# Kernel tuning notes

Hardware: AMD Instinct MI355X
Metric: run time of the kernel (lower is better)

The kernel has to match this reference:

```python
import jax, jax.numpy as jnp
import numpy as np
from functools import partial

D_MODEL, D_STATE, D_CONV, EXPAND = 1024, 16, 4, 2
D_INNER = D_MODEL * EXPAND
B_SZ, L = 4, 2048


def setup_inputs() -> dict:
    key = jax.random.key(0)
    ks = jax.random.split(key, 8)
    s = 0.02
    A_init = jnp.log(jnp.arange(1, D_STATE + 1, dtype=jnp.float32))
    return {
        "x": jax.random.normal(ks[0], (B_SZ, L, D_MODEL), jnp.float32),
        "norm_w": jnp.ones((D_MODEL,), jnp.float32),
        "norm_b": jnp.zeros((D_MODEL,), jnp.float32),
        "W_in": jax.random.normal(ks[1], (D_MODEL, 2 * D_INNER), jnp.float32) * s,
        "conv_w": jax.random.normal(ks[2], (D_INNER, 1, D_CONV), jnp.float32) * 0.3,
        "conv_b": jnp.zeros((D_INNER,), jnp.float32),
        "A_log": jnp.broadcast_to(A_init, (D_INNER, D_STATE)).copy(),
        "W_b": jax.random.normal(ks[3], (D_INNER, D_STATE), jnp.float32) * s,
        "W_c": jax.random.normal(ks[4], (D_INNER, D_STATE), jnp.float32) * s,
        "W_delta": jax.random.normal(ks[5], (D_INNER, D_INNER), jnp.float32) * s,
        "b_delta": jnp.zeros((D_INNER,), jnp.float32),
        "D_param": jnp.ones((D_INNER,), jnp.float32),
        "W_out": jax.random.normal(ks[6], (D_INNER, D_MODEL), jnp.float32) * s,
    }


def _layernorm(x, w, b, eps=1e-5):
    mu = jnp.mean(x, axis=-1, keepdims=True)
    var = jnp.mean(jnp.square(x - mu), axis=-1, keepdims=True)
    return (x - mu) * jax.lax.rsqrt(var + eps) * w + b


def reference(x, norm_w, norm_b, W_in, conv_w, conv_b, A_log, W_b, W_c,
              W_delta, b_delta, D_param, W_out):
    residual = x
    xn = _layernorm(x, norm_w, norm_b)
    xz = jnp.einsum('bld,de->ble', xn, W_in)  # [B, L, 2*D_inner]
    x_path, z = jnp.split(xz, 2, axis=-1)

    # depthwise causal conv1d (torch pads both sides K-1 then slices [:L] == left-pad K-1)
    xc = jnp.moveaxis(x_path, 1, 2)  # [B, D_inner, L]
    xc = jax.lax.conv_general_dilated(
        xc, conv_w, window_strides=(1,), padding=[(D_CONV - 1, 0)],
        dimension_numbers=('NCH', 'OIH', 'NCH'), feature_group_count=D_INNER)
    xc = xc + conv_b[None, :, None]
    x_path = jax.nn.silu(jnp.moveaxis(xc, 2, 1))  # [B, L, D_inner]

    Bm = jnp.einsum('bld,dn->bln', x_path, W_b)   # [B, L, N]
    Cm = jnp.einsum('bld,dn->bln', x_path, W_c)   # [B, L, N]
    delta = jax.nn.softplus(jnp.einsum('bld,de->ble', x_path, W_delta) + b_delta)
    A = -jnp.exp(A_log)  # [D_inner, N]

    def step(h, inp):
        xt, dt, Bt, Ct = inp  # xt,dt: [B,D]; Bt,Ct: [B,N]
        A_bar = jnp.exp(dt[..., None] * A)              # [B, D, N]
        h = A_bar * h + (dt * xt)[..., None] * Bt[:, None, :]
        y = jnp.einsum('bdn,bn->bd', h, Ct) + D_param * xt
        return h, y

    h0 = jnp.zeros((x.shape[0], D_INNER, D_STATE), x_path.dtype)
    xs = (jnp.moveaxis(x_path, 1, 0), jnp.moveaxis(delta, 1, 0),
          jnp.moveaxis(Bm, 1, 0), jnp.moveaxis(Cm, 1, 0))
    _, ys = jax.lax.scan(step, h0, xs)           # ys: [L, B, D_inner]
    y = jnp.moveaxis(ys, 0, 1)                   # [B, L, D_inner]

    return jnp.einsum('bld,de->ble', y * jax.nn.silu(z), W_out) + residual
```

## Files before the change

kernel.cpp:

```cpp
#include <hip/hip_runtime.h>
#include <hip/hip_bf16.h>

#define D_MODEL 1024
#define D_STATE 16
#define D_INNER 2048
#define BSZ     4
#define SEQ     2048
#define NTOK    (BSZ*SEQ)
#define NBIG    2176
#define NCH     16
#define TC      128

typedef __attribute__((ext_vector_type(8))) short short8;
typedef __attribute__((ext_vector_type(4))) float floatx4;

__device__ __forceinline__ ushort bf2us(float f)
{
    union { __hip_bfloat16 h; ushort u; } c;
    c.h = __float2bfloat16(f);
    return c.u;
}
__device__ __forceinline__ float us2f(ushort u)
{
    union { uint u; float f; } c;
    c.u = ((uint)u) << 16;
    return c.f;
}
__device__ __forceinline__ uint pk2(float a, float b)
{
    return (uint)bf2us(a) | ((uint)bf2us(b) << 16);
}
__device__ __forceinline__ float blo(uint u) { return __uint_as_float(u << 16); }
__device__ __forceinline__ float bhi(uint u) { return __uint_as_float(u & 0xffff0000u); }
__device__ __forceinline__ float softplus_f(float v)
{
    return (v > 20.f) ? v : __logf(1.f + __expf(v));
}

__device__ __forceinline__ void load_lds16(const __hip_bfloat16* g, __hip_bfloat16* l)
{
    __builtin_amdgcn_global_load_lds(
        (const __attribute__((address_space(1))) char*)g,
        (__attribute__((address_space(3))) char*)l, 16, 0, 0);
}

__global__ __launch_bounds__(256) void ln_kernel(
    const float* __restrict__ x, const float* __restrict__ w,
    const float* __restrict__ bvec, __hip_bfloat16* __restrict__ out)
{
    int token = blockIdx.x;
    int tid = threadIdx.x;
    const float4 v = ((const float4*)(x + (size_t)token * D_MODEL))[tid];
    float s  = v.x + v.y + v.z + v.w;
    float sq = v.x*v.x + v.y*v.y + v.z*v.z + v.w*v.w;
#pragma unroll
    for (int o = 32; o; o >>= 1) { s += __shfl_down(s, o, 64); sq += __shfl_down(sq, o, 64); }
    __shared__ float red[8];
    int wid = tid >> 6;
    if ((tid & 63) == 0) { red[wid] = s; red[wid + 4] = sq; }
    __syncthreads();
    s  = red[0] + red[1] + red[2] + red[3];
    sq = red[4] + red[5] + red[6] + red[7];
    float mu  = s * (1.f / D_MODEL);
    float var = sq * (1.f / D_MODEL) - mu * mu;
    float rs  = rsqrtf(var + 1e-5f);
    float4 wv = ((const float4*)w)[tid];
    float4 bv = ((const float4*)bvec)[tid];
    union { ushort4 u; __hip_bfloat16 h[4]; } p;
    p.h[0] = __float2bfloat16((v.x - mu) * rs * wv.x + bv.x);
    p.h[1] = __float2bfloat16((v.y - mu) * rs * wv.y + bv.y);
    p.h[2] = __float2bfloat16((v.z - mu) * rs * wv.z + bv.z);
    p.h[3] = __float2bfloat16((v.w - mu) * rs * wv.w + bv.w);
    ((ushort4*)(out + (size_t)token * D_MODEL))[tid] = p.u;
}

__global__ __launch_bounds__(256) void transpose_cast(
    const float* __restrict__ src, __hip_bfloat16* __restrict__ dst,
    int R, int C, int dstStride, int dstRowOff)
{
    __shared__ float tile[32][33];
    int tx = threadIdx.x, ty = threadIdx.y;
    int bx = blockIdx.x, by = blockIdx.y;
#pragma unroll
    for (int i = 0; i < 4; ++i) {
        int r = by * 32 + ty + i * 8;
        int c = bx * 32 + tx;
        if (r < R && c < C) tile[ty + i * 8][tx] = src[(size_t)r * C + c];
    }
    __syncthreads();
#pragma unroll
    for (int i = 0; i < 4; ++i) {
        int c = bx * 32 + ty + i * 8;
        int r = by * 32 + tx;
        if (c < C && r < R)
            dst[(size_t)(dstRowOff + c) * dstStride + r] = __float2bfloat16(tile[tx][ty + i * 8]);
    }
}

__global__ __launch_bounds__(256) void zero_fill(uint4* __restrict__ p, int n)
{
    int i = blockIdx.x * 256 + threadIdx.x;
    if (i < n) { uint4 z = {0, 0, 0, 0}; p[i] = z; }
}

template <int MODE>
__global__ __launch_bounds__(256) void gemm_bt(
    const __hip_bfloat16* __restrict__ A, const __hip_bfloat16* __restrict__ BT,
    int M, int N, int K,
    float* __restrict__ outF,
    __hip_bfloat16* __restrict__ outB1, __hip_bfloat16* __restrict__ outB2,
    const float* __restrict__ extra)
{
    __shared__ __align__(16) __hip_bfloat16 As[128 * 64];
    __shared__ __align__(16) __hip_bfloat16 Bs[128 * 64];
    int tid = threadIdx.x;
    int m0 = blockIdx.x * 128;
    int n0 = blockIdx.y * 128;
    int wv = tid >> 6, lane = tid & 63;
    int wm = (wv >> 1) * 64, wn = (wv & 1) * 64;
    int lr = lane & 15, lq = lane >> 4;

    int srow = wv * 8 + (lane >> 3);
    int scg  = (lane & 7) ^ (lane >> 3);
    const __hip_bfloat16* Ag = A  + (size_t)(m0 + srow) * K + scg * 8;
    const __hip_bfloat16* Bg = BT + (size_t)(n0 + srow) * K + scg * 8;
    __hip_bfloat16* AsW = As + (wv * 8) * 64;
    __hip_bfloat16* BsW = Bs + (wv * 8) * 64;

    int swz = lq ^ (lr & 7);

    floatx4 acc[4][4] = {};

    for (int k0 = 0; k0 < K; k0 += 64) {
        __syncthreads();
#pragma unroll
        for (int i = 0; i < 4; ++i) {
            load_lds16(Ag + (size_t)(i * 32) * K + k0, AsW + i * 32 * 64);
            load_lds16(Bg + (size_t)(i * 32) * K + k0, BsW + i * 32 * 64);
        }
        __syncthreads();
#pragma unroll
        for (int kk = 0; kk < 2; ++kk) {
            int cofs = (swz ^ (kk << 2)) * 8;
            short8 af[4], bf[4];
#pragma unroll
            for (int mi = 0; mi < 4; ++mi)
                af[mi] = *(const short8*)(As + (wm + mi * 16 + lr) * 64 + cofs);
#pragma unroll
            for (int ni = 0; ni < 4; ++ni)
                bf[ni] = *(const short8*)(Bs + (wn + ni * 16 + lr) * 64 + cofs);
#pragma unroll
            for (int mi = 0; mi < 4; ++mi)
#pragma unroll
                for (int ni = 0; ni < 4; ++ni)
                    acc[mi][ni] = __builtin_amdgcn_mfma_f32_16x16x32_bf16(af[mi], bf[ni], acc[mi][ni], 0, 0, 0);
        }
    }

#pragma unroll
    for (int mi = 0; mi < 4; ++mi)
#pragma unroll
        for (int ni = 0; ni < 4; ++ni)
#pragma unroll
            for (int r = 0; r < 4; ++r) {
                int rg = m0 + wm + mi * 16 + lq * 4 + r;
                int cg = n0 + wn + ni * 16 + lr;
                float v = acc[mi][ni][r];
                if (MODE == 1) {
                    if (cg < D_INNER) {
                        outB1[(size_t)rg * D_INNER + cg] = __float2bfloat16(v);
                    } else {
                        float sv = v / (1.f + __expf(-v));
                        outB2[(size_t)rg * D_INNER + (cg - D_INNER)] = __float2bfloat16(sv);
                    }
                } else if (MODE == 2) {
                    if (cg < D_INNER) {
                        outB1[(size_t)rg * D_INNER + cg] = __float2bfloat16(softplus_f(v + extra[cg]));
                    } else if (cg < D_INNER + 32) {
                        outB2[(size_t)rg * 32 + (cg - D_INNER)] = __float2bfloat16(v);
                    }
                } else {
                    outF[(size_t)rg * D_MODEL + cg] = v + extra[(size_t)rg * D_MODEL + cg];
                }
            }
}

__global__ __launch_bounds__(256) void conv_silu(
    const __hip_bfloat16* __restrict__ xin, const float* __restrict__ cw,
    const float* __restrict__ cb, __hip_bfloat16* __restrict__ xp)
{
    int gid = blockIdx.x * 256 + threadIdx.x;
    int d = gid & (D_INNER - 1);
    int rest = gid >> 11;
    int b = rest & 3;
    int ch = rest >> 2;
    int t0 = ch * 64;
    float w0 = cw[d * 4 + 0], w1 = cw[d * 4 + 1], w2 = cw[d * 4 + 2], w3 = cw[d * 4 + 3];
    float bias = cb[d];
    const __hip_bfloat16* base = xin + (size_t)b * SEQ * D_INNER + d;
    __hip_bfloat16* ob = xp + (size_t)b * SEQ * D_INNER + d;
    float xm3 = (t0 >= 3) ? __bfloat162float(base[(size_t)(t0 - 3) * D_INNER]) : 0.f;
    float xm2 = (t0 >= 2) ? __bfloat162float(base[(size_t)(t0 - 2) * D_INNER]) : 0.f;
    float xm1 = (t0 >= 1) ? __bfloat162float(base[(size_t)(t0 - 1) * D_INNER]) : 0.f;
#pragma unroll 4
    for (int t = t0; t < t0 + 64; ++t) {
        float xcur = __bfloat162float(base[(size_t)t * D_INNER]);
        float v = bias + w0 * xm3 + w1 * xm2 + w2 * xm1 + w3 * xcur;
        float sv = v / (1.f + __expf(-v));
        ob[(size_t)t * D_INNER] = __float2bfloat16(sv);
        xm3 = xm2; xm2 = xm1; xm1 = xcur;
    }
}


#define LOAD_A16() \
    const float4* Ar = (const float4*)(A_log + (size_t)d * D_STATE); \
    float4 aA = Ar[0], aB = Ar[1], aC = Ar[2], aD = Ar[3]; \
    float A0 = -__expf(aA.x), A1 = -__expf(aA.y), A2 = -__expf(aA.z), A3 = -__expf(aA.w); \
    float A4 = -__expf(aB.x), A5 = -__expf(aB.y), A6 = -__expf(aB.z), A7 = -__expf(aB.w); \
    float A8 = -__expf(aC.x), A9 = -__expf(aC.y), A10 = -__expf(aC.z), A11 = -__expf(aC.w); \
    float A12 = -__expf(aD.x), A13 = -__expf(aD.y), A14 = -__expf(aD.z), A15 = -__expf(aD.w)

#define UNPACK16(P, r0, r1) \
    float P##0 = blo(r0.x), P##1 = bhi(r0.x), P##2 = blo(r0.y), P##3 = bhi(r0.y); \
    float P##4 = blo(r0.z), P##5 = bhi(r0.z), P##6 = blo(r0.w), P##7 = bhi(r0.w); \
    float P##8 = blo(r1.x), P##9 = bhi(r1.x), P##10 = blo(r1.y), P##11 = bhi(r1.y); \
    float P##12 = blo(r1.z), P##13 = bhi(r1.z), P##14 = blo(r1.w), P##15 = bhi(r1.w)

__global__ __launch_bounds__(256) void scan_p1(
    const ushort* __restrict__ dtb, const ushort* __restrict__ xpb,
    const ushort* __restrict__ BC, const float* __restrict__ A_log,
    ushort* __restrict__ hloc, ushort* __restrict__ prod)
{
    int gid = blockIdx.x * 256 + threadIdx.x;
    int d  = gid & (D_INNER - 1);
    int ch = (gid >> 11) & (NCH - 1);
    int b  = gid >> 15;
    LOAD_A16();
    float h0 = 0.f, h1 = 0.f, h2 = 0.f, h3 = 0.f, h4 = 0.f, h5 = 0.f, h6 = 0.f, h7 = 0.f;
    float h8 = 0.f, h9 = 0.f, h10 = 0.f, h11 = 0.f, h12 = 0.f, h13 = 0.f, h14 = 0.f, h15 = 0.f;
    float dtsum = 0.f;
    size_t mBase = (size_t)b * SEQ + (size_t)ch * TC;
    const ushort* dtp = dtb + mBase * D_INNER + d;
    const ushort* xpp = xpb + mBase * D_INNER + d;
    const uint4*  bcp = (const uint4*)(BC + mBase * 32);
    for (int t = 0; t < TC; ++t) {
        float dt = us2f(dtp[(size_t)t * D_INNER]);
        float xt = us2f(xpp[(size_t)t * D_INNER]);
        uint4 r0 = bcp[t * 4 + 0];
        uint4 r1 = bcp[t * 4 + 1];
        float dtx = dt * xt;
        dtsum += dt;
        UNPACK16(B, r0, r1);
        h0  = __expf(dt * A0)  * h0  + dtx * B0;
        h1  = __expf(dt * A1)  * h1  + dtx * B1;
        h2  = __expf(dt * A2)  * h2  + dtx * B2;
        h3  = __expf(dt * A3)  * h3  + dtx * B3;
        h4  = __expf(dt * A4)  * h4  + dtx * B4;
        h5  = __expf(dt * A5)  * h5  + dtx * B5;
        h6  = __expf(dt * A6)  * h6  + dtx * B6;
        h7  = __expf(dt * A7)  * h7  + dtx * B7;
        h8  = __expf(dt * A8)  * h8  + dtx * B8;
        h9  = __expf(dt * A9)  * h9  + dtx * B9;
        h10 = __expf(dt * A10) * h10 + dtx * B10;
        h11 = __expf(dt * A11) * h11 + dtx * B11;
        h12 = __expf(dt * A12) * h12 + dtx * B12;
        h13 = __expf(dt * A13) * h13 + dtx * B13;
        h14 = __expf(dt * A14) * h14 + dtx * B14;
        h15 = __expf(dt * A15) * h15 + dtx * B15;
    }
    size_t idx = ((size_t)(b * NCH + ch) * D_INNER + d) * D_STATE;
    uint4 ho, h2v, po, p2v;
    ho.x  = pk2(h0, h1);   ho.y  = pk2(h2, h3);
    ho.z  = pk2(h4, h5);   ho.w  = pk2(h6, h7);
    h2v.x = pk2(h8, h9);   h2v.y = pk2(h10, h11);
    h2v.z = pk2(h12, h13); h2v.w = pk2(h14, h15);
    po.x  = pk2(__expf(dtsum * A0),  __expf(dtsum * A1));
    po.y  = pk2(__expf(dtsum * A2),  __expf(dtsum * A3));
    po.z  = pk2(__expf(dtsum * A4),  __expf(dtsum * A5));
    po.w  = pk2(__expf(dtsum * A6),  __expf(dtsum * A7));
    p2v.x = pk2(__expf(dtsum * A8),  __expf(dtsum * A9));
    p2v.y = pk2(__expf(dtsum * A10), __expf(dtsum * A11));
    p2v.z = pk2(__expf(dtsum * A12), __expf(dtsum * A13));
    p2v.w = pk2(__expf(dtsum * A14), __expf(dtsum * A15));
    ((uint4*)(hloc + idx))[0] = ho; ((uint4*)(hloc + idx))[1] = h2v;
    ((uint4*)(prod + idx))[0] = po; ((uint4*)(prod + idx))[1] = p2v;
}

__global__ __launch_bounds__(256) void scan_mid(
    ushort* __restrict__ hloc, const ushort* __restrict__ prod)
{
    int gid = blockIdx.x * 256 + threadIdx.x;
    int n = gid & 15, d = (gid >> 4) & (D_INNER - 1), b = gid >> 15;
    float h = 0.f;
#pragma unroll
    for (int ch = 0; ch < NCH; ++ch) {
        size_t idx = ((size_t)(b * NCH + ch) * D_INNER + d) * D_STATE + n;
        float old = us2f(hloc[idx]);
        float p   = us2f(prod[idx]);
        hloc[idx] = bf2us(h);
        h = old + p * h;
    }
}

__global__ __launch_bounds__(256) void scan_p2(
    const ushort* __restrict__ dtb, const ushort* __restrict__ xpb,
    const ushort* __restrict__ BC, const float* __restrict__ A_log,
    const float* __restrict__ D_param, const ushort* __restrict__ hin,
    ushort* __restrict__ zio)
{
    int gid = blockIdx.x * 256 + threadIdx.x;
    int d  = gid & (D_INNER - 1);
    int ch = (gid >> 11) & (NCH - 1);
    int b  = gid >> 15;
    LOAD_A16();
    float Dp = D_param[d];
    size_t idx = ((size_t)(b * NCH + ch) * D_INNER + d) * D_STATE;
    uint4 hr0 = ((const uint4*)(hin + idx))[0];
    uint4 hr1 = ((const uint4*)(hin + idx))[1];
    float h0 = blo(hr0.x), h1 = bhi(hr0.x), h2 = blo(hr0.y), h3 = bhi(hr0.y);
    float h4 = blo(hr0.z), h5 = bhi(hr0.z), h6 = blo(hr0.w), h7 = bhi(hr0.w);
    float h8 = blo(hr1.x), h9 = bhi(hr1.x), h10 = blo(hr1.y), h11 = bhi(hr1.y);
    float h12 = blo(hr1.z), h13 = bhi(hr1.z), h14 = blo(hr1.w), h15 = bhi(hr1.w);
    size_t mBase = (size_t)b * SEQ + (size_t)ch * TC;
    const ushort* dtp = dtb + mBase * D_INNER + d;
    const ushort* xpp = xpb + mBase * D_INNER + d;
    const uint4*  bcp = (const uint4*)(BC + mBase * 32);
    ushort* zp = zio + mBase * D_INNER + d;
    for (int t = 0; t < TC; ++t) {
        float dt = us2f(dtp[(size_t)t * D_INNER]);
        float xt = us2f(xpp[(size_t)t * D_INNER]);
        uint4 r0 = bcp[t * 4 + 0];
        uint4 r1 = bcp[t * 4 + 1];
        uint4 r2 = bcp[t * 4 + 2];
        uint4 r3 = bcp[t * 4 + 3];
        UNPACK16(B, r0, r1);
        UNPACK16(C, r2, r3);
        float dtx = dt * xt;
        float y = Dp * xt;
        h0  = __expf(dt * A0)  * h0  + dtx * B0;   y += h0  * C0;
        h1  = __expf(dt * A1)  * h1  + dtx * B1;   y += h1  * C1;
        h2  = __expf(dt * A2)  * h2  + dtx * B2;   y += h2  * C2;
        h3  = __expf(dt * A3)  * h3  + dtx * B3;   y += h3  * C3;
        h4  = __expf(dt * A4)  * h4  + dtx * B4;   y += h4  * C4;
        h5  = __expf(dt * A5)  * h5  + dtx * B5;   y += h5  * C5;
        h6  = __expf(dt * A6)  * h6  + dtx * B6;   y += h6  * C6;
        h7  = __expf(dt * A7)  * h7  + dtx * B7;   y += h7  * C7;
        h8  = __expf(dt * A8)  * h8  + dtx * B8;   y += h8  * C8;
        h9  = __expf(dt * A9)  * h9  + dtx * B9;   y += h9  * C9;
        h10 = __expf(dt * A10) * h10 + dtx * B10;  y += h10 * C10;
        h11 = __expf(dt * A11) * h11 + dtx * B11;  y += h11 * C11;
        h12 = __expf(dt * A12) * h12 + dtx * B12;  y += h12 * C12;
        h13 = __expf(dt * A13) * h13 + dtx * B13;  y += h13 * C13;
        h14 = __expf(dt * A14) * h14 + dtx * B14;  y += h14 * C14;
        h15 = __expf(dt * A15) * h15 + dtx * B15;  y += h15 * C15;
        float z = us2f(zp[(size_t)t * D_INNER]);
        zp[(size_t)t * D_INNER] = bf2us(y * z);
    }
}

extern "C" void kernel_launch(void* const* d_in, const int* in_sizes, int n_in,
                              void* d_out, int out_size, void* d_ws, size_t ws_size,
                              hipStream_t stream)
{
    const float* x       = (const float*)d_in[0];
    const float* norm_w  = (const float*)d_in[1];
    const float* norm_b  = (const float*)d_in[2];
    const float* W_in    = (const float*)d_in[3];
    const float* conv_w  = (const float*)d_in[4];
    const float* conv_b  = (const float*)d_in[5];
    const float* A_log   = (const float*)d_in[6];
    const float* W_b     = (const float*)d_in[7];
    const float* W_c     = (const float*)d_in[8];
    const float* W_delta = (const float*)d_in[9];
    const float* b_delta = (const float*)d_in[10];
    const float* D_param = (const float*)d_in[11];
    const float* W_out   = (const float*)d_in[12];
    float* out = (float*)d_out;

    char* ws = (char*)d_ws;
    char* R1 = ws;
    char* R2 = R1 + (size_t)33554432;
    char* R3 = R2 + (size_t)33554432;
    char* R4 = R3 + (size_t)33554432;
    char* R5 = R4 + (size_t)8912896;

    __hip_bfloat16* xnb  = (__hip_bfloat16*)R1;
    __hip_bfloat16* wT1  = (__hip_bfloat16*)(R1 + 16777216);
    __hip_bfloat16* xp   = (__hip_bfloat16*)R1;
    __hip_bfloat16* xraw = (__hip_bfloat16*)R2;
    __hip_bfloat16* dtb  = (__hip_bfloat16*)R2;
    __hip_bfloat16* wT3  = (__hip_bfloat16*)R2;
    __hip_bfloat16* zio  = (__hip_bfloat16*)R3;
    __hip_bfloat16* wT2  = (__hip_bfloat16*)R4;
    ushort*         hloc = (ushort*)R4;
    ushort*         prodb= (ushort*)(R4 + 4194304);
    __hip_bfloat16* BCb  = (__hip_bfloat16*)R5;

    ln_kernel<<<NTOK, 256, 0, stream>>>(x, norm_w, norm_b, xnb);

    transpose_cast<<<dim3(128, 32), dim3(32, 8), 0, stream>>>(W_in, wT1, 1024, 4096, 1024, 0);

    gemm_bt<1><<<dim3(NTOK / 128, 4096 / 128), 256, 0, stream>>>(
        xnb, wT1, NTOK, 4096, 1024, nullptr, xraw, zio, nullptr);

    transpose_cast<<<dim3(64, 64), dim3(32, 8), 0, stream>>>(W_delta, wT2, 2048, 2048, 2048, 0);
    transpose_cast<<<dim3(1, 64),  dim3(32, 8), 0, stream>>>(W_b,     wT2, 2048, 16,   2048, 2048);
    transpose_cast<<<dim3(1, 64),  dim3(32, 8), 0, stream>>>(W_c,     wT2, 2048, 16,   2048, 2064);
    zero_fill<<<96, 256, 0, stream>>>((uint4*)(wT2 + (size_t)2080 * 2048), 24576);

    conv_silu<<<1024, 256, 0, stream>>>(xraw, conv_w, conv_b, xp);

    gemm_bt<2><<<dim3(NTOK / 128, NBIG / 128), 256, 0, stream>>>(
        xp, wT2, NTOK, NBIG, 2048, nullptr, dtb, BCb, b_delta);

    scan_p1<<<512, 256, 0, stream>>>((const ushort*)dtb, (const ushort*)xp,
                                     (const ushort*)BCb, A_log, hloc, prodb);
    scan_mid<<<512, 256, 0, stream>>>(hloc, prodb);
    scan_p2<<<512, 256, 0, stream>>>((const ushort*)dtb, (const ushort*)xp,
                                     (const ushort*)BCb, A_log, D_param, hloc,
                                     (ushort*)zio);

    transpose_cast<<<dim3(32, 64), dim3(32, 8), 0, stream>>>(W_out, wT3, 2048, 1024, 2048, 0);

    gemm_bt<3><<<dim3(NTOK / 128, D_MODEL / 128), 256, 0, stream>>>(
        zio, wT3, NTOK, D_MODEL, 2048, out, nullptr, nullptr, x);

    (void)in_sizes; (void)n_in; (void)out_size; (void)ws_size;
}
```

Measured before the change: 582.5 us.

## Fuse weight prep kernels, fold chunk-prefix into scan_p2, prefetch scan inputs

```diff
diff --git a/kernel.cpp b/kernel.cpp
--- a/kernel.cpp
+++ b/kernel.cpp
@@ -74,13 +74,11 @@
     ((ushort4*)(out + (size_t)token * D_MODEL))[tid] = p.u;
 }
 
-__global__ __launch_bounds__(256) void transpose_cast(
+__device__ __forceinline__ void tr_body(
     const float* __restrict__ src, __hip_bfloat16* __restrict__ dst,
-    int R, int C, int dstStride, int dstRowOff)
+    int R, int C, int dstStride, int dstRowOff, int bx, int by, int tx, int ty)
 {
     __shared__ float tile[32][33];
-    int tx = threadIdx.x, ty = threadIdx.y;
-    int bx = blockIdx.x, by = blockIdx.y;
 #pragma unroll
     for (int i = 0; i < 4; ++i) {
         int r = by * 32 + ty + i * 8;
@@ -97,14 +95,39 @@
     }
 }
 
-__global__ __launch_bounds__(256) void zero_fill(uint4* __restrict__ p, int n)
-{
-    int i = blockIdx.x * 256 + threadIdx.x;
-    if (i < n) { uint4 z = {0, 0, 0, 0}; p[i] = z; }
+__global__ __launch_bounds__(256) void transpose_cast(
+    const float* __restrict__ src, __hip_bfloat16* __restrict__ dst,
+    int R, int C, int dstStride, int dstRowOff)
+{
+    tr_body(src, dst, R, C, dstStride, dstRowOff,
+            blockIdx.x, blockIdx.y, threadIdx.x, threadIdx.y);
+}
+
+__global__ __launch_bounds__(256) void prep_w(
+    const float* __restrict__ W_in, const float* __restrict__ W_delta,
+    const float* __restrict__ W_b, const float* __restrict__ W_c,
+    __hip_bfloat16* __restrict__ wT1, __hip_bfloat16* __restrict__ wT2)
+{
+    int s = blockIdx.x;
+    int tx = threadIdx.x, ty = threadIdx.y;
+    if (s < 4096) {
+        tr_body(W_in, wT1, 1024, 4096, 1024, 0, s & 127, s >> 7, tx, ty);
+    } else if (s < 8192) {
+        int q = s - 4096;
+        tr_body(W_delta, wT2, 2048, 2048, 2048, 0, q & 63, q >> 6, tx, ty);
+    } else if (s < 8256) {
+        tr_body(W_b, wT2, 2048, 16, 2048, 2048, 0, s - 8192, tx, ty);
+    } else if (s < 8320) {
+        tr_body(W_c, wT2, 2048, 16, 2048, 2064, 0, s - 8256, tx, ty);
+    } else {
+        int i = (s - 8320) * 256 + ty * 32 + tx;
+        uint4 z = {0, 0, 0, 0};
+        ((uint4*)(wT2 + (size_t)2080 * 2048))[i] = z;
+    }
 }
 
 template <int MODE>
-__global__ __launch_bounds__(256) void gemm_bt(
+__device__ __forceinline__ void gemm_body(
     const __hip_bfloat16* __restrict__ A, const __hip_bfloat16* __restrict__ BT,
     int M, int N, int K,
     float* __restrict__ outF,
@@ -185,6 +208,27 @@
             }
 }
 
+__global__ __launch_bounds__(256) void gemm_xz(
+    const __hip_bfloat16* __restrict__ A, const __hip_bfloat16* __restrict__ BT,
+    int M, int N, int K, float* __restrict__ outF,
+    __hip_bfloat16* __restrict__ o1, __hip_bfloat16* __restrict__ o2,
+    const float* __restrict__ extra)
+{ gemm_body<1>(A, BT, M, N, K, outF, o1, o2, extra); }
+
+__global__ __launch_bounds__(256) void gemm_dbc(
+    const __hip_bfloat16* __restrict__ A, const __hip_bfloat16* __restrict__ BT,
+    int M, int N, int K, float* __restrict__ outF,
+    __hip_bfloat16* __restrict__ o1, __hip_bfloat16* __restrict__ o2,
+    const float* __restrict__ extra)
+{ gemm_body<2>(A, BT, M, N, K, outF, o1, o2, extra); }
+
+__global__ __launch_bounds__(256) void gemm_out(
+    const __hip_bfloat16* __restrict__ A, const __hip_bfloat16* __restrict__ BT,
+    int M, int N, int K, float* __restrict__ outF,
+    __hip_bfloat16* __restrict__ o1, __hip_bfloat16* __restrict__ o2,
+    const float* __restrict__ extra)
+{ gemm_body<3>(A, BT, M, N, K, outF, o1, o2, extra); }
+
 __global__ __launch_bounds__(256) void conv_silu(
     const __hip_bfloat16* __restrict__ xin, const float* __restrict__ cw,
     const float* __restrict__ cb, __hip_bfloat16* __restrict__ xp)
@@ -227,6 +271,26 @@
     float P##8 = blo(r1.x), P##9 = bhi(r1.x), P##10 = blo(r1.y), P##11 = bhi(r1.y); \
     float P##12 = blo(r1.z), P##13 = bhi(r1.z), P##14 = blo(r1.w), P##15 = bhi(r1.w)
 
+#define SCAN_STEP_B() do { \
+    float dtx = dt * xt; \
+    h0  = __expf(dt * A0)  * h0  + dtx * B0; \
+    h1  = __expf(dt * A1)  * h1  + dtx * B1; \
+    h2  = __expf(dt * A2)  * h2  + dtx * B2; \
+    h3  = __expf(dt * A3)  * h3  + dtx * B3; \
+    h4  = __expf(dt * A4)  * h4  + dtx * B4; \
+    h5  = __expf(dt * A5)  * h5  + dtx * B5; \
+    h6  = __expf(dt * A6)  * h6  + dtx * B6; \
+    h7  = __expf(dt * A7)  * h7  + dtx * B7; \
+    h8  = __expf(dt * A8)  * h8  + dtx * B8; \
+    h9  = __expf(dt * A9)  * h9  + dtx * B9; \
+    h10 = __expf(dt * A10) * h10 + dtx * B10; \
+    h11 = __expf(dt * A11) * h11 + dtx * B11; \
+    h12 = __expf(dt * A12) * h12 + dtx * B12; \
+    h13 = __expf(dt * A13) * h13 + dtx * B13; \
+    h14 = __expf(dt * A14) * h14 + dtx * B14; \
+    h15 = __expf(dt * A15) * h15 + dtx * B15; \
+} while (0)
+
 __global__ __launch_bounds__(256) void scan_p1(
     const ushort* __restrict__ dtb, const ushort* __restrict__ xpb,
     const ushort* __restrict__ BC, const float* __restrict__ A_log,
@@ -244,30 +308,25 @@
     const ushort* dtp = dtb + mBase * D_INNER + d;
     const ushort* xpp = xpb + mBase * D_INNER + d;
     const uint4*  bcp = (const uint4*)(BC + mBase * 32);
-    for (int t = 0; t < TC; ++t) {
-        float dt = us2f(dtp[(size_t)t * D_INNER]);
-        float xt = us2f(xpp[(size_t)t * D_INNER]);
-        uint4 r0 = bcp[t * 4 + 0];
-        uint4 r1 = bcp[t * 4 + 1];
-        float dtx = dt * xt;
+    float dt = us2f(dtp[0]);
+    float xt = us2f(xpp[0]);
+    uint4 r0 = bcp[0], r1 = bcp[1];
+    for (int t = 0; t < TC - 1; ++t) {
+        float dt_n = us2f(dtp[(size_t)(t + 1) * D_INNER]);
+        float xt_n = us2f(xpp[(size_t)(t + 1) * D_INNER]);
+        uint4 r0_n = bcp[(t + 1) * 4 + 0];
+        uint4 r1_n = bcp[(t + 1) * 4 + 1];
+        {
+            UNPACK16(B, r0, r1);
+            dtsum += dt;
+            SCAN_STEP_B();
+        }
+        dt = dt_n; xt = xt_n; r0 = r0_n; r1 = r1_n;
+    }
+    {
+        UNPACK16(B, r0, r1);
         dtsum += dt;
-        UNPACK16(B, r0, r1);
-        h0  = __expf(dt * A0)  * h0  + dtx * B0;
-        h1  = __expf(dt * A1)  * h1  + dtx * B1;
-        h2  = __expf(dt * A2)  * h2  + dtx * B2;
-        h3  = __expf(dt * A3)  * h3  + dtx * B3;
-        h4  = __expf(dt * A4)  * h4  + dtx * B4;
-        h5  = __expf(dt * A5)  * h5  + dtx * B5;
-        h6  = __expf(dt * A6)  * h6  + dtx * B6;
-        h7  = __expf(dt * A7)  * h7  + dtx * B7;
-        h8  = __expf(dt * A8)  * h8  + dtx * B8;
-        h9  = __expf(dt * A9)  * h9  + dtx * B9;
-        h10 = __expf(dt * A10) * h10 + dtx * B10;
-        h11 = __expf(dt * A11) * h11 + dtx * B11;
-        h12 = __expf(dt * A12) * h12 + dtx * B12;
-        h13 = __expf(dt * A13) * h13 + dtx * B13;
-        h14 = __expf(dt * A14) * h14 + dtx * B14;
-        h15 = __expf(dt * A15) * h15 + dtx * B15;
+        SCAN_STEP_B();
     }
     size_t idx = ((size_t)(b * NCH + ch) * D_INNER + d) * D_STATE;
     uint4 ho, h2v, po, p2v;
@@ -287,27 +346,11 @@
     ((uint4*)(prod + idx))[0] = po; ((uint4*)(prod + idx))[1] = p2v;
 }
 
-__global__ __launch_bounds__(256) void scan_mid(
-    ushort* __restrict__ hloc, const ushort* __restrict__ prod)
-{
-    int gid = blockIdx.x * 256 + threadIdx.x;
-    int n = gid & 15, d = (gid >> 4) & (D_INNER - 1), b = gid >> 15;
-    float h = 0.f;
-#pragma unroll
-    for (int ch = 0; ch < NCH; ++ch) {
-        size_t idx = ((size_t)(b * NCH + ch) * D_INNER + d) * D_STATE + n;
-        float old = us2f(hloc[idx]);
-        float p   = us2f(prod[idx]);
-        hloc[idx] = bf2us(h);
-        h = old + p * h;
-    }
-}
-
 __global__ __launch_bounds__(256) void scan_p2(
     const ushort* __restrict__ dtb, const ushort* __restrict__ xpb,
     const ushort* __restrict__ BC, const float* __restrict__ A_log,
-    const float* __restrict__ D_param, const ushort* __restrict__ hin,
-    ushort* __restrict__ zio)
+    const float* __restrict__ D_param, const ushort* __restrict__ hloc,
+    const ushort* __restrict__ prod, ushort* __restrict__ zio)
 {
     int gid = blockIdx.x * 256 + threadIdx.x;
     int d  = gid & (D_INNER - 1);
@@ -315,47 +358,67 @@
     int b  = gid >> 15;
     LOAD_A16();
     float Dp = D_param[d];
-    size_t idx = ((size_t)(b * NCH + ch) * D_INNER + d) * D_STATE;
-    uint4 hr0 = ((const uint4*)(hin + idx))[0];
-    uint4 hr1 = ((const uint4*)(hin + idx))[1];
-    float h0 = blo(hr0.x), h1 = bhi(hr0.x), h2 = blo(hr0.y), h3 = bhi(hr0.y);
-    float h4 = blo(hr0.z), h5 = bhi(hr0.z), h6 = blo(hr0.w), h7 = bhi(hr0.w);
-    float h8 = blo(hr1.x), h9 = bhi(hr1.x), h10 = blo(hr1.y), h11 = bhi(hr1.y);
-    float h12 = blo(hr1.z), h13 = bhi(hr1.z), h14 = blo(hr1.w), h15 = bhi(hr1.w);
+    float h0 = 0.f, h1 = 0.f, h2 = 0.f, h3 = 0.f, h4 = 0.f, h5 = 0.f, h6 = 0.f, h7 = 0.f;
+    float h8 = 0.f, h9 = 0.f, h10 = 0.f, h11 = 0.f, h12 = 0.f, h13 = 0.f, h14 = 0.f, h15 = 0.f;
+    for (int j = 0; j < ch; ++j) {
+        size_t jdx = ((size_t)(b * NCH + j) * D_INNER + d) * D_STATE;
+        uint4 a0 = ((const uint4*)(hloc + jdx))[0];
+        uint4 a1 = ((const uint4*)(hloc + jdx))[1];
+        uint4 q0 = ((const uint4*)(prod + jdx))[0];
+        uint4 q1 = ((const uint4*)(prod + jdx))[1];
+        h0  = blo(a0.x) + blo(q0.x) * h0;   h1  = bhi(a0.x) + bhi(q0.x) * h1;
+        h2  = blo(a0.y) + blo(q0.y) * h2;   h3  = bhi(a0.y) + bhi(q0.y) * h3;
+        h4  = blo(a0.z) + blo(q0.z) * h4;   h5  = bhi(a0.z) + bhi(q0.z) * h5;
+        h6  = blo(a0.w) + blo(q0.w) * h6;   h7  = bhi(a0.w) + bhi(q0.w) * h7;
+        h8  = blo(a1.x) + blo(q1.x) * h8;   h9  = bhi(a1.x) + bhi(q1.x) * h9;
+        h10 = blo(a1.y) + blo(q1.y) * h10;  h11 = bhi(a1.y) + bhi(q1.y) * h11;
+        h12 = blo(a1.z) + blo(q1.z) * h12;  h13 = bhi(a1.z) + bhi(q1.z) * h13;
+        h14 = blo(a1.w) + blo(q1.w) * h14;  h15 = bhi(a1.w) + bhi(q1.w) * h15;
+    }
     size_t mBase = (size_t)b * SEQ + (size_t)ch * TC;
     const ushort* dtp = dtb + mBase * D_INNER + d;
     const ushort* xpp = xpb + mBase * D_INNER + d;
     const uint4*  bcp = (const uint4*)(BC + mBase * 32);
     ushort* zp = zio + mBase * D_INNER + d;
+    float dt = us2f(dtp[0]);
+    float xt = us2f(xpp[0]);
+    uint4 r0 = bcp[0], r1 = bcp[1], r2 = bcp[2], r3 = bcp[3];
     for (int t = 0; t < TC; ++t) {
-        float dt = us2f(dtp[(size_t)t * D_INNER]);
-        float xt = us2f(xpp[(size_t)t * D_INNER]);
-        uint4 r0 = bcp[t * 4 + 0];
-        uint4 r1 = bcp[t * 4 + 1];
-        uint4 r2 = bcp[t * 4 + 2];
-        uint4 r3 = bcp[t * 4 + 3];
-        UNPACK16(B, r0, r1);
-        UNPACK16(C, r2, r3);
-        float dtx = dt * xt;
-        float y = Dp * xt;
-        h0  = __expf(dt * A0)  * h0  + dtx * B0;   y += h0  * C0;
-        h1  = __expf(dt * A1)  * h1  + dtx * B1;   y += h1  * C1;
-        h2  = __expf(dt * A2)  * h2  + dtx * B2;   y += h2  * C2;
-        h3  = __expf(dt * A3)  * h3  + dtx * B3;   y += h3  * C3;
-        h4  = __expf(dt * A4)  * h4  + dtx * B4;   y += h4  * C4;
-        h5  = __expf(dt * A5)  * h5  + dtx * B5;   y += h5  * C5;
-        h6  = __expf(dt * A6)  * h6  + dtx * B6;   y += h6  * C6;
-        h7  = __expf(dt * A7)  * h7  + dtx * B7;   y += h7  * C7;
-        h8  = __expf(dt * A8)  * h8  + dtx * B8;   y += h8  * C8;
-        h9  = __expf(dt * A9)  * h9  + dtx * B9;   y += h9  * C9;
-        h10 = __expf(dt * A10) * h10 + dtx * B10;  y += h10 * C10;
-        h11 = __expf(dt * A11) * h11 + dtx * B11;  y += h11 * C11;
-        h12 = __expf(dt * A12) * h12 + dtx * B12;  y += h12 * C12;
-        h13 = __expf(dt * A13) * h13 + dtx * B13;  y += h13 * C13;
-        h14 = __expf(dt * A14) * h14 + dtx * B14;  y += h14 * C14;
-        h15 = __expf(dt * A15) * h15 + dtx * B15;  y += h15 * C15;
-        float z = us2f(zp[(size_t)t * D_INNER]);
-        zp[(size_t)t * D_INNER] = bf2us(y * z);
+        float dt_n = 0.f, xt_n = 0.f;
+        uint4 r0_n = {0,0,0,0}, r1_n = {0,0,0,0}, r2_n = {0,0,0,0}, r3_n = {0,0,0,0};
+        if (t < TC - 1) {
+            dt_n = us2f(dtp[(size_t)(t + 1) * D_INNER]);
+            xt_n = us2f(xpp[(size_t)(t + 1) * D_INNER]);
+            r0_n = bcp[(t + 1) * 4 + 0];
+            r1_n = bcp[(t + 1) * 4 + 1];
+            r2_n = bcp[(t + 1) * 4 + 2];
+            r3_n = bcp[(t + 1) * 4 + 3];
+        }
+        {
+            UNPACK16(B, r0, r1);
+            UNPACK16(C, r2, r3);
+            float dtx = dt * xt;
+            float y = Dp * xt;
+            h0  = __expf(dt * A0)  * h0  + dtx * B0;   y += h0  * C0;
+            h1  = __expf(dt * A1)  * h1  + dtx * B1;   y += h1  * C1;
+            h2  = __expf(dt * A2)  * h2  + dtx * B2;   y += h2  * C2;
+            h3  = __expf(dt * A3)  * h3  + dtx * B3;   y += h3  * C3;
+            h4  = __expf(dt * A4)  * h4  + dtx * B4;   y += h4  * C4;
+            h5  = __expf(dt * A5)  * h5  + dtx * B5;   y += h5  * C5;
+            h6  = __expf(dt * A6)  * h6  + dtx * B6;   y += h6  * C6;
+            h7  = __expf(dt * A7)  * h7  + dtx * B7;   y += h7  * C7;
+            h8  = __expf(dt * A8)  * h8  + dtx * B8;   y += h8  * C8;
+            h9  = __expf(dt * A9)  * h9  + dtx * B9;   y += h9  * C9;
+            h10 = __expf(dt * A10) * h10 + dtx * B10;  y += h10 * C10;
+            h11 = __expf(dt * A11) * h11 + dtx * B11;  y += h11 * C11;
+            h12 = __expf(dt * A12) * h12 + dtx * B12;  y += h12 * C12;
+            h13 = __expf(dt * A13) * h13 + dtx * B13;  y += h13 * C13;
+            h14 = __expf(dt * A14) * h14 + dtx * B14;  y += h14 * C14;
+            h15 = __expf(dt * A15) * h15 + dtx * B15;  y += h15 * C15;
+            float z = us2f(zp[(size_t)t * D_INNER]);
+            zp[(size_t)t * D_INNER] = bf2us(y * z);
+        }
+        dt = dt_n; xt = xt_n; r0 = r0_n; r1 = r1_n; r2 = r2_n; r3 = r3_n;
     }
 }
 
@@ -399,31 +462,25 @@
 
     ln_kernel<<<NTOK, 256, 0, stream>>>(x, norm_w, norm_b, xnb);
 
-    transpose_cast<<<dim3(128, 32), dim3(32, 8), 0, stream>>>(W_in, wT1, 1024, 4096, 1024, 0);
-
-    gemm_bt<1><<<dim3(NTOK / 128, 4096 / 128), 256, 0, stream>>>(
+    prep_w<<<8416, dim3(32, 8), 0, stream>>>(W_in, W_delta, W_b, W_c, wT1, wT2);
+
+    gemm_xz<<<dim3(NTOK / 128, 4096 / 128), 256, 0, stream>>>(
         xnb, wT1, NTOK, 4096, 1024, nullptr, xraw, zio, nullptr);
 
-    transpose_cast<<<dim3(64, 64), dim3(32, 8), 0, stream>>>(W_delta, wT2, 2048, 2048, 2048, 0);
-    transpose_cast<<<dim3(1, 64),  dim3(32, 8), 0, stream>>>(W_b,     wT2, 2048, 16,   2048, 2048);
-    transpose_cast<<<dim3(1, 64),  dim3(32, 8), 0, stream>>>(W_c,     wT2, 2048, 16,   2048, 2064);
-    zero_fill<<<96, 256, 0, stream>>>((uint4*)(wT2 + (size_t)2080 * 2048), 24576);
-
     conv_silu<<<1024, 256, 0, stream>>>(xraw, conv_w, conv_b, xp);
 
-    gemm_bt<2><<<dim3(NTOK / 128, NBIG / 128), 256, 0, stream>>>(
+    gemm_dbc<<<dim3(NTOK / 128, NBIG / 128), 256, 0, stream>>>(
         xp, wT2, NTOK, NBIG, 2048, nullptr, dtb, BCb, b_delta);
 
     scan_p1<<<512, 256, 0, stream>>>((const ushort*)dtb, (const ushort*)xp,
                                      (const ushort*)BCb, A_log, hloc, prodb);
-    scan_mid<<<512, 256, 0, stream>>>(hloc, prodb);
     scan_p2<<<512, 256, 0, stream>>>((const ushort*)dtb, (const ushort*)xp,
-                                     (const ushort*)BCb, A_log, D_param, hloc,
-                                     (ushort*)zio);
+                                     (const ushort*)BCb, A_log, D_param,
+                                     hloc, prodb, (ushort*)zio);
 
     transpose_cast<<<dim3(32, 64), dim3(32, 8), 0, stream>>>(W_out, wT3, 2048, 1024, 2048, 0);
 
-    gemm_bt<3><<<dim3(NTOK / 128, D_MODEL / 128), 256, 0, stream>>>(
+    gemm_out<<<dim3(NTOK / 128, D_MODEL / 128), 256, 0, stream>>>(
         zio, wT3, NTOK, D_MODEL, 2048, out, nullptr, nullptr, x);
 
     (void)in_sizes; (void)n_in; (void)out_size; (void)ws_size;
```

New measurement: 574.5 us. No clear change (-1.4%).
